# Performance work log

Hardware: AMD Instinct MI355X
Metric: run time of the kernel (lower is better)

## Reference

```python
import jax, jax.numpy as jnp
import numpy as np

B, H, W = 2, 32, 128
HW = H * W
N, C = 4096, 64
KQ, KN = 32, 16          # nsample_q, nsample
DIST = 10.0              # neighbor distance threshold
NEG = -1e10


def _knn(q, p, k):
    # q: (B,M,3), p: (B,N,3) -> idx (B,M,k), sqdist (B,M,k)
    sqd = jnp.sum((q[:, :, None, :] - p[:, None, :, :]) ** 2, axis=-1)
    neg, idx = jax.lax.top_k(-sqd, k)
    return idx, -neg


def _gather(p, idx):
    # p: (B,N,C), idx: (B,M,K) -> (B,M,K,C)
    return jax.vmap(lambda a, i: a[i])(p, idx)


def _norm_feat(x):
    # per-point channel normalization, torch.std default is unbiased (ddof=1)
    m = jnp.mean(x, axis=-1, keepdims=True)
    s = jnp.clip(jnp.std(x, axis=-1, keepdims=True, ddof=1), 1e-12)
    return (x - m) / s


def _conv(x, w, b, g, e):
    # 1x1 conv + BatchNorm (track_running_stats=False -> batch stats) + LeakyReLU(0.1)
    y = jnp.einsum('bnkc,cd->bnkd', x, w) + b
    mu = y.mean(axis=(0, 1, 2), keepdims=True)
    var = y.var(axis=(0, 1, 2), keepdims=True)
    y = (y - mu) * jax.lax.rsqrt(var + 1e-5) * g + e
    return jnp.where(y > 0, y, 0.1 * y)


def setup_inputs() -> dict:
    key = jax.random.key(0)
    ks = jax.random.split(key, 20)
    inp = {
        'xyz_proj_raw': jax.random.normal(ks[0], (B, H, W, 3), jnp.float32),
        'warped_xyz': jax.random.normal(ks[1], (B, HW, 3), jnp.float32),
        'warped_points': jax.random.normal(ks[2], (B, HW, C), jnp.float32),
        'idx_n2': jax.random.randint(ks[3], (B, HW, 2), 0, W),
        'f2_xyz': jax.random.normal(ks[4], (B, N, 3), jnp.float32),
        'f2_points': jax.random.normal(ks[5], (B, N, C), jnp.float32),
        'lidar_z': jax.random.uniform(ks[6], (B, HW, 1), jnp.float32),
    }
    shapes = {
        'm1w0': (70, 128), 'm1w1': (128, 64), 'piw': (6, 64),
        'm2w0': (128, 64), 'm2w1': (64, 64), 'pcw': (10, 64),
        'm3w0': (192, 64), 'm3w1': (64, 64),
    }
    i = 7
    for name, shp in shapes.items():
        inp[name] = jax.random.normal(ks[i], shp, jnp.float32) * 0.05
        i += 1
        pre = name[:-2] if name[-2] == 'w' else name[:-1]
        suf = name[-1] if name[-2] == 'w' else ''
        cout = shp[1]
        inp[pre + 'b' + suf] = jnp.zeros((cout,), jnp.float32)
        inp[pre + 'g' + suf] = jnp.ones((cout,), jnp.float32)
        inp[pre + 'e' + suf] = jnp.zeros((cout,), jnp.float32)
    return inp


def reference(xyz_proj_raw, warped_xyz, warped_points, idx_n2, f2_xyz, f2_points, lidar_z,
              m1w0, m1b0, m1g0, m1e0, m1w1, m1b1, m1g1, m1e1,
              piw, pib, pig, pie,
              m2w0, m2b0, m2g0, m2e0, m2w1, m2b1, m2g1, m2e1,
              pcw, pcb, pcg, pce,
              m3w0, m3b0, m3g0, m3e0, m3w1, m3b1, m3g1, m3e1):
    # ---- stage 1: cross kNN grouping into image features ----
    idx_q, _ = _knn(warped_xyz, f2_xyz, KQ)
    qi_xyz = _gather(f2_xyz, idx_q)          # (B,HW,KQ,3)
    qi_pts = _gather(f2_points, idx_q)       # (B,HW,KQ,C)

    wxyz = warped_xyz * lidar_z              # (B,HW,3)
    pi_xyz_exp = jnp.broadcast_to(wxyz[:, :, None, :], (B, HW, KQ, 3))
    pi_pts_exp = jnp.broadcast_to(warped_points[:, :, None, :], (B, HW, KQ, C))
    pi_xyz_diff_concat = jnp.concatenate([pi_xyz_exp, qi_xyz], axis=3)  # (B,HW,KQ,6)

    pi_feat_diff = _norm_feat(pi_pts_exp) * _norm_feat(qi_pts)          # correlation
    feat = jnp.concatenate([pi_xyz_diff_concat, pi_feat_diff], axis=3)  # (B,HW,KQ,70)

    feat = _conv(feat, m1w0, m1b0, m1g0, m1e0)
    feat = _conv(feat, m1w1, m1b1, m1g1, m1e1)                          # (B,HW,KQ,64)
    pi_enc = _conv(pi_xyz_diff_concat, piw, pib, pig, pie)              # (B,HW,KQ,64)

    pi_cat = jnp.concatenate([pi_enc, feat], axis=3)
    pi_cat = _conv(pi_cat, m2w0, m2b0, m2g0, m2e0)
    pi_cat = _conv(pi_cat, m2w1, m2b1, m2g1, m2e1)
    WQ = jax.nn.softmax(pi_cat, axis=2)
    pi_feat1 = jnp.sum(WQ * feat, axis=2)                               # (B,HW,64)

    # ---- stage 2: self kNN (use_trans=False -> raw projected xyz), thresholded validity ----
    xyz_pr = xyz_proj_raw.reshape(B, HW, 3)
    idx2, sqd2 = _knn(xyz_pr, xyz_pr, KN)
    valid = (sqd2 < DIST * DIST).astype(pi_feat1.dtype)[..., None]      # (B,HW,KN,1)

    pc_xyz_g = _gather(wxyz, idx2)                                      # (B,HW,KN,3)
    pc_pts_g = _gather(pi_feat1, idx2)                                  # (B,HW,KN,64)
    pc_xyz_new = jnp.broadcast_to(wxyz[:, :, None, :], (B, HW, KN, 3))
    pc_pts_new = jnp.broadcast_to(warped_points[:, :, None, :], (B, HW, KN, C))

    pc_diff = pc_xyz_g - pc_xyz_new
    pc_euc = jnp.sqrt(jnp.sum(pc_diff * pc_diff, axis=3, keepdims=True) + 1e-20)
    pc_xyz_cat = jnp.concatenate([pc_xyz_new, pc_xyz_g, pc_diff, pc_euc], axis=3)  # 10ch

    pc_enc = _conv(pc_xyz_cat, pcw, pcb, pcg, pce)
    pc_cat = jnp.concatenate([pc_enc, pc_pts_new, pc_pts_g], axis=-1)   # (B,HW,KN,192)
    pc_cat = _conv(pc_cat, m3w0, m3b0, m3g0, m3e0)
    pc_cat = _conv(pc_cat, m3w1, m3b1, m3g1, m3e1)

    pc_cat = pc_cat * valid + NEG * (1.0 - valid)
    WP = jax.nn.softmax(pc_cat, axis=2)
    out = jnp.sum(WP * pc_pts_g, axis=2)                                # (B,HW,64)
    return out.reshape(B, H, W, -1)
```

## Files before the change

### kernel.cpp

```cpp
#include <hip/hip_runtime.h>
#include <math.h>

constexpr int Bn  = 2;
constexpr int HWn = 4096;
constexpr int Nn  = 4096;
constexpr int KQn = 32;
constexpr int KNn = 16;
constexpr float INV_R1 = 1.0f/262144.0f;
constexpr float INV_R2 = 1.0f/131072.0f;

typedef _Float16 f16x8 __attribute__((ext_vector_type(8)));
typedef float    f32x4 __attribute__((ext_vector_type(4)));

__device__ __forceinline__ float wred64(float v){
  #pragma unroll
  for (int m = 32; m > 0; m >>= 1) v += __shfl_xor(v, m, 64);
  return v;
}
__device__ __forceinline__ float leakyf(float v){ return v > 0.f ? v : 0.1f*v; }

__device__ __forceinline__ void bn_param(const float* st, int c, float inv_n,
                                         const float* g, const float* e,
                                         float& sc, float& sh){
  float mu  = st[c]*inv_n;
  float var = st[128+c]*inv_n - mu*mu;
  float s   = g[c]*rsqrtf(var + 1e-5f);
  sc = s; sh = e[c] - mu*s;
}

__device__ __forceinline__ void build_x70(int row,
    const float* __restrict__ wxyz, const float* __restrict__ f2_xyz,
    const float* __restrict__ normW, const float* __restrict__ normF2,
    const int* __restrict__ idxq, float* x){
  int p = row >> 5;
  int b = p >> 12;
  int idx = idxq[row];
  const float* wx = wxyz + (size_t)p*3;
  const float* fx = f2_xyz + ((size_t)b*Nn + idx)*3;
  x[0]=wx[0]; x[1]=wx[1]; x[2]=wx[2];
  x[3]=fx[0]; x[4]=fx[1]; x[5]=fx[2];
  const float4* nw = (const float4*)(normW  + (size_t)p*64);
  const float4* nf = (const float4*)(normF2 + ((size_t)b*Nn + idx)*64);
  #pragma unroll
  for (int c=0;c<16;c++){
    float4 a = nw[c], q = nf[c];
    x[6+4*c+0]=a.x*q.x; x[6+4*c+1]=a.y*q.y; x[6+4*c+2]=a.z*q.z; x[6+4*c+3]=a.w*q.w;
  }
}

__device__ __forceinline__ void build_x10(int row,
    const float* __restrict__ wxyz, const int* __restrict__ idx2, float* x){
  int p = row >> 4, b = p >> 12;
  int idx = idx2[row];
  const float* nw = wxyz + (size_t)p*3;
  const float* gw = wxyz + ((size_t)b*HWn + idx)*3;
  float n0=nw[0],n1=nw[1],n2=nw[2];
  float g0=gw[0],g1=gw[1],g2=gw[2];
  float d0=g0-n0, d1=g1-n1, d2=g2-n2;
  x[0]=n0;x[1]=n1;x[2]=n2; x[3]=g0;x[4]=g1;x[5]=g2;
  x[6]=d0;x[7]=d1;x[8]=d2; x[9]=sqrtf(d0*d0+d1*d1+d2*d2+1e-20f);
}

__global__ __launch_bounds__(256) void k_prep(
    const float* __restrict__ warped_xyz, const float* __restrict__ lidar_z,
    const float* __restrict__ warped_points, const float* __restrict__ f2_points,
    const float* __restrict__ m1w0, const float* __restrict__ m1w1,
    const float* __restrict__ piw, const float* __restrict__ pcw,
    const float* __restrict__ m2w0, const float* __restrict__ m2w1,
    const float* __restrict__ m3w0, const float* __restrict__ m3w1,
    float* __restrict__ wxyz, float* __restrict__ normW, float* __restrict__ normF2,
    float* __restrict__ piwT, float* __restrict__ pcwT,
    _Float16* __restrict__ w1h, _Float16* __restrict__ w2h,
    _Float16* __restrict__ w3h, _Float16* __restrict__ w4h,
    _Float16* __restrict__ w5h, _Float16* __restrict__ w6h)
{
  int blk = blockIdx.x, tid = threadIdx.x;
  if (blk < 4096){
    int lane = tid & 63;
    int p = blk*4 + (tid >> 6);
    const float* src; float* dst;
    if (p < Bn*HWn){ src = warped_points + (size_t)p*64; dst = normW + (size_t)p*64; }
    else { int q = p - Bn*HWn; src = f2_points + (size_t)q*64; dst = normF2 + (size_t)q*64; }
    float x = src[lane];
    float m = wred64(x) * (1.f/64.f);
    float d = x - m;
    float ss = wred64(d*d);
    float s = fmaxf(sqrtf(ss*(1.f/63.f)), 1e-12f);
    dst[lane] = d / s;
  } else if (blk < 4192){
    int e = (blk-4096)*256 + tid;
    wxyz[e] = warped_xyz[e] * lidar_z[e/3];
  } else if (blk < 4196){
    int e = (blk-4192)*256 + tid;
    if (e < 384){ piwT[(e & 63)*6  + (e >> 6)] = piw[e]; }
    else if (e < 1024){ int f = e-384; pcwT[(f & 63)*10 + (f >> 6)] = pcw[f]; }
  } else {
    int e = (blk-4196)*256 + tid;
    if (e < 12288){
      int j = e/96, k = e - j*96;
      w1h[e] = (k < 70) ? (_Float16)m1w0[k*128 + j] : (_Float16)0.f;
    } else if (e < 20480){
      int f = e - 12288; int d = f >> 7, c = f & 127;
      w2h[f] = (_Float16)m1w1[c*64 + d];
    } else if (e < 28672){
      int f = e - 20480; int d = f >> 7, c = f & 127;
      w3h[f] = (_Float16)m2w0[c*64 + d];
    } else if (e < 32768){
      int f = e - 28672; int d = f >> 6, c = f & 63;
      w4h[f] = (_Float16)m2w1[c*64 + d];
    } else if (e < 45056){
      int f = e - 32768; int d = f/192, c = f - 192*d;
      w5h[f] = (_Float16)m3w0[c*64 + d];
    } else {
      int f = e - 45056; int d = f >> 6, c = f & 63;
      w6h[f] = (_Float16)m3w1[c*64 + d];
    }
  }
}

template<int K, bool WRITE_VALID>
__global__ __launch_bounds__(256) void k_knn(
    const float* __restrict__ qpts, const float* __restrict__ pts,
    int* __restrict__ oidx, float* __restrict__ ovalid)
{
  __shared__ int hist[4*256];
  __shared__ int wsum[4];
  __shared__ unsigned int redm[4], redM[4];
  __shared__ unsigned int sh_sel;
  __shared__ int sh_rem, sh_cls, cnt_lt, cnt_eq;
  int b = blockIdx.x >> 12;
  int qi = blockIdx.x & 4095;
  int tid = threadIdx.x;
  int lane = tid & 63, wv = tid >> 6;
  const float* qp = qpts + ((size_t)(b*HWn+qi))*3;
  float qx=qp[0], qy=qp[1], qz=qp[2];
  const float* pb = pts + (size_t)b*Nn*3;
  unsigned int key[16];
  {
    const float4* pb4 = (const float4*)(pb + (size_t)tid*48);
    float4 v[12];
    #pragma unroll
    for (int i=0;i<12;i++) v[i] = pb4[i];
    const float* f = (const float*)v;
    #pragma unroll
    for (int i=0;i<16;i++){
      float dx = __fsub_rn(qx, f[i*3+0]);
      float dy = __fsub_rn(qy, f[i*3+1]);
      float dz = __fsub_rn(qz, f[i*3+2]);
      float d2 = __fadd_rn(__fadd_rn(__fmul_rn(dx,dx), __fmul_rn(dy,dy)), __fmul_rn(dz,dz));
      key[i] = __float_as_uint(d2);
    }
  }
  unsigned int mn = key[0], mx = key[0];
  #pragma unroll
  for (int i=1;i<16;i++){ mn = min(mn, key[i]); mx = max(mx, key[i]); }
  #pragma unroll
  for (int m=32;m>0;m>>=1){
    mn = min(mn, (unsigned int)__shfl_xor((int)mn, m, 64));
    mx = max(mx, (unsigned int)__shfl_xor((int)mx, m, 64));
  }
  if (lane == 0){ redm[wv] = mn; redM[wv] = mx; }
  if (tid == 0){ cnt_lt = 0; cnt_eq = 0; }
  __syncthreads();
  mn = min(min(redm[0],redm[1]), min(redm[2],redm[3]));
  mx = max(max(redM[0],redM[1]), max(redM[2],redM[3]));
  unsigned int R = mx - mn;
  int L = (R == 0u) ? 0 : (31 - __clz(R));
  int shift = (L > 7) ? (L - 7) : 0;
  unsigned int dmask = 255u;

  unsigned int active = 0xFFFFu, below = 0u;
  int rem = K;
  for (;;){
    __syncthreads();
    #pragma unroll
    for (int j=0;j<4;j++) hist[j*256 + tid] = 0;
    __syncthreads();
    #pragma unroll
    for (int i=0;i<16;i++){
      if (active & (1u<<i))
        atomicAdd(&hist[wv*256 + (int)(((key[i]-mn) >> shift) & dmask)], 1);
    }
    __syncthreads();
    int h = hist[tid] + hist[256+tid] + hist[512+tid] + hist[768+tid];
    int pref = h;
    #pragma unroll
    for (int m=1;m<64;m<<=1){ int t = __shfl_up(pref, m, 64); if (lane >= m) pref += t; }
    if (lane == 63) wsum[wv] = pref;
    __syncthreads();
    int off = 0;
    #pragma unroll
    for (int i=0;i<3;i++) if (i < wv) off += wsum[i];
    pref += off;
    if (pref >= rem && (pref - h) < rem){
      sh_sel = (unsigned int)tid;
      sh_rem = rem - (pref - h);
      sh_cls = h;
    }
    __syncthreads();
    unsigned int sel = sh_sel; rem = sh_rem; int cls = sh_cls;
    #pragma unroll
    for (int i=0;i<16;i++){
      if (active & (1u<<i)){
        unsigned int d = ((key[i]-mn) >> shift) & dmask;
        if (d < sel) below |= (1u<<i);
        if (d != sel) active &= ~(1u<<i);
      }
    }
    if (cls == rem || shift == 0) break;
    int w = (shift < 8) ? shift : 8;
    shift -= w;
    dmask = (w == 8) ? 255u : ((1u<<w) - 1u);
  }
  size_t obase = ((size_t)(b*HWn+qi))*K;
  int nless = K - rem;
  const unsigned int U100 = __float_as_uint(100.0f);
  #pragma unroll
  for (int i=0;i<16;i++){
    if (below & (1u<<i)){
      int s = atomicAdd(&cnt_lt, 1);
      oidx[obase+s] = tid*16 + i;
      if constexpr (WRITE_VALID) ovalid[obase+s] = (key[i] < U100) ? 1.f : 0.f;
    } else if (active & (1u<<i)){
      int s = atomicAdd(&cnt_eq, 1);
      if (s < rem){
        oidx[obase+nless+s] = tid*16 + i;
        if constexpr (WRITE_VALID) ovalid[obase+nless+s] = (key[i] < U100) ? 1.f : 0.f;
      }
    }
  }
}

__global__ __launch_bounds__(256) void k_build_stats(
    const float* __restrict__ wxyz, const float* __restrict__ f2_xyz,
    const float* __restrict__ normW, const float* __restrict__ normF2,
    const int* __restrict__ idxq, const int* __restrict__ idx2,
    const _Float16* __restrict__ w1h,
    _Float16* __restrict__ X1, float* stats, float* __restrict__ gram)
{
  __shared__ float ssum[128], sssq[128];
  __shared__ float sacc[66];
  int blk = blockIdx.x, tid = threadIdx.x, lane = tid & 63;
  if (blk < 1024){
    int row = blk*256 + tid;
    {
      float x[70];
      build_x70(row, wxyz, f2_xyz, normW, normF2, idxq, x);
      unsigned int* d32 = (unsigned int*)(X1 + (size_t)row*96);
      union { unsigned int u; _Float16 h[2]; } pk;
      #pragma unroll
      for (int c=0;c<35;c++){
        pk.h[0] = (_Float16)x[2*c]; pk.h[1] = (_Float16)x[2*c+1];
        d32[c] = pk.u;
      }
      #pragma unroll
      for (int c=35;c<48;c++) d32[c] = 0u;
    }
    if (tid < 128){ ssum[tid]=0.f; sssq[tid]=0.f; }
    __syncthreads();
    int wave = tid >> 6;
    int quad = lane >> 4, n16 = lane & 15;
    float r1[8], r2[8];
    #pragma unroll
    for (int i=0;i<8;i++){ r1[i]=0.f; r2[i]=0.f; }
    for (int t=0;t<4;t++){
      int m0 = blk*256 + t*64 + wave*16;
      const _Float16* xr = X1 + (size_t)(m0 + n16)*96 + quad*8;
      f16x8 a0 = *(const f16x8*)(xr);
      f16x8 a1 = *(const f16x8*)(xr + 32);
      f16x8 a2 = *(const f16x8*)(xr + 64);
      #pragma unroll
      for (int nt = 0; nt < 8; nt++){
        const _Float16* wr = w1h + (size_t)(nt*16 + n16)*96 + quad*8;
        f16x8 b0 = *(const f16x8*)(wr);
        f16x8 b1 = *(const f16x8*)(wr + 32);
        f16x8 b2 = *(const f16x8*)(wr + 64);
        f32x4 acc = {0.f,0.f,0.f,0.f};
        acc = __builtin_amdgcn_mfma_f32_16x16x32_f16(a0, b0, acc, 0,0,0);
        acc = __builtin_amdgcn_mfma_f32_16x16x32_f16(a1, b1, acc, 0,0,0);
        acc = __builtin_amdgcn_mfma_f32_16x16x32_f16(a2, b2, acc, 0,0,0);
        float s1 = acc[0]+acc[1]+acc[2]+acc[3];
        float s2 = acc[0]*acc[0]+acc[1]*acc[1]+acc[2]*acc[2]+acc[3]*acc[3];
        s1 += __shfl_xor(s1, 16, 64); s1 += __shfl_xor(s1, 32, 64);
        s2 += __shfl_xor(s2, 16, 64); s2 += __shfl_xor(s2, 32, 64);
        r1[nt] += s1; r2[nt] += s2;
      }
    }
    if (quad == 0){
      #pragma unroll
      for (int nt=0;nt<8;nt++){
        atomicAdd(&ssum[nt*16+n16], r1[nt]); atomicAdd(&sssq[nt*16+n16], r2[nt]);
      }
    }
    __syncthreads();
    if (tid < 128){ atomicAdd(&stats[tid], ssum[tid]); atomicAdd(&stats[128+tid], sssq[tid]); }
  } else if (blk < 1088){
    float a[28];
    #pragma unroll
    for (int q=0;q<28;q++) a[q]=0.f;
    int g = (blk-1024)*256 + tid;
    for (int s=0;s<16;s++){
      int row = g + s*16384;
      int p = row >> 5, b = p >> 12;
      int idx = idxq[row];
      const float* wx = wxyz + (size_t)p*3;
      const float* fx = f2_xyz + ((size_t)b*Nn + idx)*3;
      float xt[7] = {wx[0],wx[1],wx[2],fx[0],fx[1],fx[2],1.f};
      int q=0;
      #pragma unroll
      for (int i=0;i<7;i++)
        #pragma unroll
        for (int j=i;j<7;j++) a[q++] += xt[i]*xt[j];
    }
    if (tid < 28) sacc[tid]=0.f;
    __syncthreads();
    #pragma unroll
    for (int q=0;q<28;q++){
      float v = wred64(a[q]);
      if (lane==0) atomicAdd(&sacc[q], v);
    }
    __syncthreads();
    if (tid < 28) atomicAdd(&gram[tid], sacc[tid]);
  } else {
    float a[66];
    #pragma unroll
    for (int q=0;q<66;q++) a[q]=0.f;
    int g = (blk-1088)*256 + tid;
    for (int s=0;s<16;s++){
      int row = g + s*8192;
      float x[10];
      build_x10(row, wxyz, idx2, x);
      float xt[11] = {x[0],x[1],x[2],x[3],x[4],x[5],x[6],x[7],x[8],x[9],1.f};
      int q=0;
      #pragma unroll
      for (int i=0;i<11;i++)
        #pragma unroll
        for (int j=i;j<11;j++) a[q++] += xt[i]*xt[j];
    }
    if (tid < 66) sacc[tid]=0.f;
    __syncthreads();
    #pragma unroll
    for (int q=0;q<66;q++){
      float v = wred64(a[q]);
      if (lane==0) atomicAdd(&sacc[q], v);
    }
    __syncthreads();
    if (tid < 66) atomicAdd(&gram[32+tid], sacc[tid]);
  }
}

__global__ __launch_bounds__(128) void k_gram_fin(
    const float* __restrict__ gram,
    const float* __restrict__ piw, const float* __restrict__ pib,
    const float* __restrict__ pcw, const float* __restrict__ pcb,
    float* stats)
{
  int tid = threadIdx.x;
  if (tid < 64){
    int c = tid;
    float wt[7];
    #pragma unroll
    for (int i=0;i<6;i++) wt[i] = piw[i*64+c];
    wt[6] = pib[c];
    const float* G = gram;
    float sum=0.f, ssq=0.f;
    #pragma unroll
    for (int i=0;i<7;i++){
      int offi = i*7 - (i*(i-1))/2;
      sum += wt[i]*G[offi + (6-i)];
      #pragma unroll
      for (int j=0;j<7;j++){
        int ii = i<j? i : j, jj = i<j? j : i;
        int o = ii*7 - (ii*(ii-1))/2 + (jj-ii);
        ssq += wt[i]*wt[j]*G[o];
      }
    }
    stats[2*256+c] = sum; stats[2*256+128+c] = ssq;
  } else {
    int c = tid-64;
    float wt[11];
    #pragma unroll
    for (int i=0;i<10;i++) wt[i] = pcw[i*64+c];
    wt[10] = pcb[c];
    const float* G = gram + 32;
    float sum=0.f, ssq=0.f;
    #pragma unroll
    for (int i=0;i<11;i++){
      int offi = i*11 - (i*(i-1))/2;
      sum += wt[i]*G[offi + (10-i)];
      #pragma unroll
      for (int j=0;j<11;j++){
        int ii = i<j? i : j, jj = i<j? j : i;
        int o = ii*11 - (ii*(ii-1))/2 + (jj-ii);
        ssq += wt[i]*wt[j]*G[o];
      }
    }
    stats[5*256+c] = sum; stats[5*256+128+c] = ssq;
  }
}

__global__ __launch_bounds__(256) void k_mfma_m1(
    const _Float16* __restrict__ X1, const _Float16* __restrict__ w1h,
    const _Float16* __restrict__ w2h,
    const float* __restrict__ m1g0, const float* __restrict__ m1e0,
    float* stats, _Float16* __restrict__ y2h)
{
  __shared__ _Float16 st[64*136];
  __shared__ float sc1[128], sh1[128], ssum[64], sssq[64];
  int tid = threadIdx.x;
  if (tid < 128){
    float s,h; bn_param(stats, tid, INV_R1, m1g0, m1e0, s, h);
    sc1[tid]=s; sh1[tid]=h;
  }
  if (tid < 64){ ssum[tid]=0.f; sssq[tid]=0.f; }
  __syncthreads();
  int wave = tid >> 6, lane = tid & 63;
  int quad = lane >> 4, n16 = lane & 15;
  float r1[4], r2[4];
  #pragma unroll
  for (int i=0;i<4;i++){ r1[i]=0.f; r2[i]=0.f; }
  for (int t=0;t<4;t++){
    int m0 = blockIdx.x*256 + t*64 + wave*16;
    const _Float16* xr = X1 + (size_t)(m0 + n16)*96 + quad*8;
    f16x8 a0 = *(const f16x8*)(xr);
    f16x8 a1 = *(const f16x8*)(xr + 32);
    f16x8 a2 = *(const f16x8*)(xr + 64);
    #pragma unroll
    for (int nt = 0; nt < 8; nt++){
      const _Float16* wr = w1h + (size_t)(nt*16 + n16)*96 + quad*8;
      f16x8 b0 = *(const f16x8*)(wr);
      f16x8 b1 = *(const f16x8*)(wr + 32);
      f16x8 b2 = *(const f16x8*)(wr + 64);
      f32x4 acc = {0.f,0.f,0.f,0.f};
      acc = __builtin_amdgcn_mfma_f32_16x16x32_f16(a0, b0, acc, 0,0,0);
      acc = __builtin_amdgcn_mfma_f32_16x16x32_f16(a1, b1, acc, 0,0,0);
      acc = __builtin_amdgcn_mfma_f32_16x16x32_f16(a2, b2, acc, 0,0,0);
      int ch = nt*16 + n16;
      float sc = sc1[ch], sh = sh1[ch];
      #pragma unroll
      for (int r=0;r<4;r++){
        float v = leakyf(acc[r]*sc + sh);
        st[(size_t)(wave*16 + quad*4 + r)*136 + ch] = (_Float16)v;
      }
    }
    __syncthreads();
    const _Float16* tr = st + (size_t)(wave*16 + n16)*136 + quad*8;
    f16x8 t0 = *(const f16x8*)(tr);
    f16x8 t1 = *(const f16x8*)(tr + 32);
    f16x8 t2 = *(const f16x8*)(tr + 64);
    f16x8 t3 = *(const f16x8*)(tr + 96);
    #pragma unroll
    for (int nt = 0; nt < 4; nt++){
      const _Float16* wr = w2h + (size_t)(nt*16 + n16)*128 + quad*8;
      f16x8 b0 = *(const f16x8*)(wr);
      f16x8 b1 = *(const f16x8*)(wr + 32);
      f16x8 b2 = *(const f16x8*)(wr + 64);
      f16x8 b3 = *(const f16x8*)(wr + 96);
      f32x4 acc = {0.f,0.f,0.f,0.f};
      acc = __builtin_amdgcn_mfma_f32_16x16x32_f16(t0, b0, acc, 0,0,0);
      acc = __builtin_amdgcn_mfma_f32_16x16x32_f16(t1, b1, acc, 0,0,0);
      acc = __builtin_amdgcn_mfma_f32_16x16x32_f16(t2, b2, acc, 0,0,0);
      acc = __builtin_amdgcn_mfma_f32_16x16x32_f16(t3, b3, acc, 0,0,0);
      int ch = nt*16 + n16;
      #pragma unroll
      for (int r=0;r<4;r++){
        int rowg = blockIdx.x*256 + t*64 + wave*16 + quad*4 + r;
        y2h[(size_t)rowg*64 + ch] = (_Float16)acc[r];
      }
      float s1 = acc[0]+acc[1]+acc[2]+acc[3];
      float s2 = acc[0]*acc[0]+acc[1]*acc[1]+acc[2]*acc[2]+acc[3]*acc[3];
      s1 += __shfl_xor(s1, 16, 64); s1 += __shfl_xor(s1, 32, 64);
      s2 += __shfl_xor(s2, 16, 64); s2 += __shfl_xor(s2, 32, 64);
      r1[nt] += s1; r2[nt] += s2;
    }
    __syncthreads();
  }
  if (quad == 0){
    #pragma unroll
    for (int nt=0;nt<4;nt++){
      atomicAdd(&ssum[nt*16+n16], r1[nt]); atomicAdd(&sssq[nt*16+n16], r2[nt]);
    }
  }
  __syncthreads();
  if (tid < 64){ atomicAdd(&stats[1*256+tid], ssum[tid]); atomicAdd(&stats[1*256+128+tid], sssq[tid]); }
}

__global__ __launch_bounds__(256) void k_mfma_m2a(
    const float* __restrict__ wxyz, const float* __restrict__ f2_xyz,
    const int* __restrict__ idxq,
    const float* __restrict__ piwT, const float* __restrict__ pib,
    const float* __restrict__ pig, const float* __restrict__ pie,
    const float* __restrict__ m1g1, const float* __restrict__ m1e1,
    const _Float16* __restrict__ y2h, const _Float16* __restrict__ w3h,
    float* stats, _Float16* __restrict__ y3h)
{
  __shared__ _Float16 su[64*136];
  __shared__ float spw[384];
  __shared__ float scp[64], shp[64], sc2[64], sh2[64], ssum[64], sssq[64];
  int tid = threadIdx.x;
  for (int d = tid; d < 384; d += 256) spw[d] = piwT[d];
  if (tid < 64){
    float s,h;
    bn_param(stats+2*256, tid, INV_R1, pig,  pie,  s, h); scp[tid]=s; shp[tid]=h;
    bn_param(stats+1*256, tid, INV_R1, m1g1, m1e1, s, h); sc2[tid]=s; sh2[tid]=h;
    ssum[tid]=0.f; sssq[tid]=0.f;
  }
  __syncthreads();
  int r = tid & 63, cg = tid >> 6;
  int wave = tid >> 6, lane = tid & 63, quad = lane >> 4, n16 = lane & 15;
  float r1[4], r2[4];
  #pragma unroll
  for (int i=0;i<4;i++){ r1[i]=0.f; r2[i]=0.f; }
  for (int t=0;t<4;t++){
    int rowg = blockIdx.x*256 + t*64 + r;
    {
      int p = rowg >> 5, b = p >> 12;
      int idx = idxq[rowg];
      const float* wx = wxyz + (size_t)p*3;
      const float* fx = f2_xyz + ((size_t)b*Nn + idx)*3;
      float x0=wx[0],x1=wx[1],x2=wx[2],x3=fx[0],x4=fx[1],x5=fx[2];
      #pragma unroll
      for (int jj=0;jj<16;jj++){
        int j = cg*16 + jj;
        const float* pw = spw + j*6;
        float e = pib[j] + x0*pw[0]+x1*pw[1]+x2*pw[2]+x3*pw[3]+x4*pw[4]+x5*pw[5];
        su[r*136 + j] = (_Float16)leakyf(e*scp[j] + shp[j]);
      }
      const f16x8* yr = (const f16x8*)(y2h + (size_t)rowg*64 + cg*16);
      f16x8 q0 = yr[0], q1 = yr[1];
      #pragma unroll
      for (int jj=0;jj<8;jj++){
        int c = cg*16 + jj;
        su[r*136 + 64 + c] = (_Float16)leakyf((float)q0[jj]*sc2[c] + sh2[c]);
      }
      #pragma unroll
      for (int jj=0;jj<8;jj++){
        int c = cg*16 + 8 + jj;
        su[r*136 + 64 + c] = (_Float16)leakyf((float)q1[jj]*sc2[c] + sh2[c]);
      }
    }
    __syncthreads();
    const _Float16* ur = su + (size_t)(wave*16 + n16)*136 + quad*8;
    f16x8 a0 = *(const f16x8*)(ur);
    f16x8 a1 = *(const f16x8*)(ur + 32);
    f16x8 a2 = *(const f16x8*)(ur + 64);
    f16x8 a3 = *(const f16x8*)(ur + 96);
    #pragma unroll
    for (int nt = 0; nt < 4; nt++){
      const _Float16* wr = w3h + (size_t)(nt*16 + n16)*128 + quad*8;
      f16x8 b0 = *(const f16x8*)(wr);
      f16x8 b1 = *(const f16x8*)(wr + 32);
      f16x8 b2 = *(const f16x8*)(wr + 64);
      f16x8 b3 = *(const f16x8*)(wr + 96);
      f32x4 acc = {0.f,0.f,0.f,0.f};
      acc = __builtin_amdgcn_mfma_f32_16x16x32_f16(a0, b0, acc, 0,0,0);
      acc = __builtin_amdgcn_mfma_f32_16x16x32_f16(a1, b1, acc, 0,0,0);
      acc = __builtin_amdgcn_mfma_f32_16x16x32_f16(a2, b2, acc, 0,0,0);
      acc = __builtin_amdgcn_mfma_f32_16x16x32_f16(a3, b3, acc, 0,0,0);
      int ch = nt*16 + n16;
      #pragma unroll
      for (int rr=0;rr<4;rr++){
        int rg = blockIdx.x*256 + t*64 + wave*16 + quad*4 + rr;
        y3h[(size_t)rg*64 + ch] = (_Float16)acc[rr];
      }
      float s1 = acc[0]+acc[1]+acc[2]+acc[3];
      float s2 = acc[0]*acc[0]+acc[1]*acc[1]+acc[2]*acc[2]+acc[3]*acc[3];
      s1 += __shfl_xor(s1, 16, 64); s1 += __shfl_xor(s1, 32, 64);
      s2 += __shfl_xor(s2, 16, 64); s2 += __shfl_xor(s2, 32, 64);
      r1[nt] += s1; r2[nt] += s2;
    }
    __syncthreads();
  }
  if (quad == 0){
    #pragma unroll
    for (int nt=0;nt<4;nt++){
      atomicAdd(&ssum[nt*16+n16], r1[nt]); atomicAdd(&sssq[nt*16+n16], r2[nt]);
    }
  }
  __syncthreads();
  if (tid < 64){ atomicAdd(&stats[3*256+tid], ssum[tid]); atomicAdd(&stats[3*256+128+tid], sssq[tid]); }
}

__global__ __launch_bounds__(256) void k_mfma_pw64(
    const _Float16* __restrict__ yin, const _Float16* __restrict__ wh,
    const float* __restrict__ g, const float* __restrict__ e,
    const float* statsIn, float* statsOut, float inv_n,
    _Float16* __restrict__ yout)
{
  __shared__ _Float16 stt[64*72];
  __shared__ float sc[64], sh[64], ssum[64], sssq[64];
  int tid = threadIdx.x;
  if (tid < 64){
    float s,h; bn_param(statsIn, tid, inv_n, g, e, s, h);
    sc[tid]=s; sh[tid]=h; ssum[tid]=0.f; sssq[tid]=0.f;
  }
  __syncthreads();
  int r = tid & 63, cg = tid >> 6;
  int wave = tid >> 6, lane = tid & 63, quad = lane >> 4, n16 = lane & 15;
  float r1[4], r2[4];
  #pragma unroll
  for (int i=0;i<4;i++){ r1[i]=0.f; r2[i]=0.f; }
  for (int t=0;t<4;t++){
    int rowg = blockIdx.x*256 + t*64 + r;
    const f16x8* yr = (const f16x8*)(yin + (size_t)rowg*64 + cg*16);
    f16x8 q0 = yr[0], q1 = yr[1];
    #pragma unroll
    for (int jj=0;jj<8;jj++){
      int c = cg*16 + jj;
      stt[r*72 + c] = (_Float16)leakyf((float)q0[jj]*sc[c] + sh[c]);
    }
    #pragma unroll
    for (int jj=0;jj<8;jj++){
      int c = cg*16 + 8 + jj;
      stt[r*72 + c] = (_Float16)leakyf((float)q1[jj]*sc[c] + sh[c]);
    }
    __syncthreads();
    const _Float16* tr = stt + (size_t)(wave*16 + n16)*72 + quad*8;
    f16x8 a0 = *(const f16x8*)(tr);
    f16x8 a1 = *(const f16x8*)(tr + 32);
    #pragma unroll
    for (int nt = 0; nt < 4; nt++){
      const _Float16* wr = wh + (size_t)(nt*16 + n16)*64 + quad*8;
      f16x8 b0 = *(const f16x8*)(wr);
      f16x8 b1 = *(const f16x8*)(wr + 32);
      f32x4 acc = {0.f,0.f,0.f,0.f};
      acc = __builtin_amdgcn_mfma_f32_16x16x32_f16(a0, b0, acc, 0,0,0);
      acc = __builtin_amdgcn_mfma_f32_16x16x32_f16(a1, b1, acc, 0,0,0);
      int ch = nt*16 + n16;
      #pragma unroll
      for (int rr=0;rr<4;rr++){
        int rg = blockIdx.x*256 + t*64 + wave*16 + quad*4 + rr;
        yout[(size_t)rg*64 + ch] = (_Float16)acc[rr];
      }
      float s1 = acc[0]+acc[1]+acc[2]+acc[3];
      float s2 = acc[0]*acc[0]+acc[1]*acc[1]+acc[2]*acc[2]+acc[3]*acc[3];
      s1 += __shfl_xor(s1, 16, 64); s1 += __shfl_xor(s1, 32, 64);
      s2 += __shfl_xor(s2, 16, 64); s2 += __shfl_xor(s2, 32, 64);
      r1[nt] += s1; r2[nt] += s2;
    }
    __syncthreads();
  }
  if (quad == 0){
    #pragma unroll
    for (int nt=0;nt<4;nt++){
      atomicAdd(&ssum[nt*16+n16], r1[nt]); atomicAdd(&sssq[nt*16+n16], r2[nt]);
    }
  }
  __syncthreads();
  if (tid < 64){ atomicAdd(&statsOut[tid], ssum[tid]); atomicAdd(&statsOut[128+tid], sssq[tid]); }
}

__global__ __launch_bounds__(256) void k_mfma_m3a(
    const float* __restrict__ wxyz, const float* __restrict__ warped_points,
    const _Float16* __restrict__ pif1h, const int* __restrict__ idx2,
    const float* __restrict__ pcwT, const float* __restrict__ pcb,
    const float* __restrict__ pcg, const float* __restrict__ pce,
    const _Float16* __restrict__ w5h,
    float* stats, _Float16* __restrict__ y5h)
{
  __shared__ _Float16 sv[64*200];
  __shared__ float spw[640];
  __shared__ float scp[64], shp[64], ssum[64], sssq[64];
  int tid = threadIdx.x;
  for (int d = tid; d < 640; d += 256) spw[d] = pcwT[d];
  if (tid < 64){
    float s,h; bn_param(stats+5*256, tid, INV_R2, pcg, pce, s, h);
    scp[tid]=s; shp[tid]=h; ssum[tid]=0.f; sssq[tid]=0.f;
  }
  __syncthreads();
  int r = tid & 63, cg = tid >> 6;
  int wave = tid >> 6, lane = tid & 63, quad = lane >> 4, n16 = lane & 15;
  float r1[4], r2[4];
  #pragma unroll
  for (int i=0;i<4;i++){ r1[i]=0.f; r2[i]=0.f; }
  for (int t=0;t<4;t++){
    int rowg = blockIdx.x*256 + t*64 + r;
    {
      int p = rowg >> 4, b = p >> 12;
      int idx = idx2[rowg];
      float x[10];
      build_x10(rowg, wxyz, idx2, x);
      #pragma unroll
      for (int jj=0;jj<16;jj++){
        int j = cg*16 + jj;
        const float* pw = spw + j*10;
        float e = pcb[j];
        #pragma unroll
        for (int i=0;i<10;i++) e += x[i]*pw[i];
        sv[r*200 + j] = (_Float16)leakyf(e*scp[j] + shp[j]);
      }
      const float4* wp = (const float4*)(warped_points + (size_t)p*64 + cg*16);
      #pragma unroll
      for (int v4=0; v4<4; v4++){
        float4 q = wp[v4];
        int c = 64 + cg*16 + v4*4;
        sv[r*200 + c + 0] = (_Float16)q.x;
        sv[r*200 + c + 1] = (_Float16)q.y;
        sv[r*200 + c + 2] = (_Float16)q.z;
        sv[r*200 + c + 3] = (_Float16)q.w;
      }
      const f16x8* pg = (const f16x8*)(pif1h + ((size_t)(b*HWn) + idx)*64 + cg*16);
      f16x8 g0 = pg[0], g1 = pg[1];
      #pragma unroll
      for (int jj=0;jj<8;jj++) sv[r*200 + 128 + cg*16 + jj] = g0[jj];
      #pragma unroll
      for (int jj=0;jj<8;jj++) sv[r*200 + 136 + cg*16 + jj] = g1[jj];
    }
    __syncthreads();
    const _Float16* vr = sv + (size_t)(wave*16 + n16)*200 + quad*8;
    f16x8 a0 = *(const f16x8*)(vr);
    f16x8 a1 = *(const f16x8*)(vr + 32);
    f16x8 a2 = *(const f16x8*)(vr + 64);
    f16x8 a3 = *(const f16x8*)(vr + 96);
    f16x8 a4 = *(const f16x8*)(vr + 128);
    f16x8 a5 = *(const f16x8*)(vr + 160);
    #pragma unroll
    for (int nt = 0; nt < 4; nt++){
      const _Float16* wr = w5h + (size_t)(nt*16 + n16)*192 + quad*8;
      f32x4 acc = {0.f,0.f,0.f,0.f};
      acc = __builtin_amdgcn_mfma_f32_16x16x32_f16(a0, *(const f16x8*)(wr),       acc, 0,0,0);
      acc = __builtin_amdgcn_mfma_f32_16x16x32_f16(a1, *(const f16x8*)(wr + 32),  acc, 0,0,0);
      acc = __builtin_amdgcn_mfma_f32_16x16x32_f16(a2, *(const f16x8*)(wr + 64),  acc, 0,0,0);
      acc = __builtin_amdgcn_mfma_f32_16x16x32_f16(a3, *(const f16x8*)(wr + 96),  acc, 0,0,0);
      acc = __builtin_amdgcn_mfma_f32_16x16x32_f16(a4, *(const f16x8*)(wr + 128), acc, 0,0,0);
      acc = __builtin_amdgcn_mfma_f32_16x16x32_f16(a5, *(const f16x8*)(wr + 160), acc, 0,0,0);
      int ch = nt*16 + n16;
      #pragma unroll
      for (int rr=0;rr<4;rr++){
        int rg = blockIdx.x*256 + t*64 + wave*16 + quad*4 + rr;
        y5h[(size_t)rg*64 + ch] = (_Float16)acc[rr];
      }
      float s1 = acc[0]+acc[1]+acc[2]+acc[3];
      float s2 = acc[0]*acc[0]+acc[1]*acc[1]+acc[2]*acc[2]+acc[3]*acc[3];
      s1 += __shfl_xor(s1, 16, 64); s1 += __shfl_xor(s1, 32, 64);
      s2 += __shfl_xor(s2, 16, 64); s2 += __shfl_xor(s2, 32, 64);
      r1[nt] += s1; r2[nt] += s2;
    }
    __syncthreads();
  }
  if (quad == 0){
    #pragma unroll
    for (int nt=0;nt<4;nt++){
      atomicAdd(&ssum[nt*16+n16], r1[nt]); atomicAdd(&sssq[nt*16+n16], r2[nt]);
    }
  }
  __syncthreads();
  if (tid < 64){ atomicAdd(&stats[6*256+tid], ssum[tid]); atomicAdd(&stats[6*256+128+tid], sssq[tid]); }
}

__global__ __launch_bounds__(256) void k_softmax1(
    const _Float16* __restrict__ y2h, const _Float16* __restrict__ y4h,
    const float* stats,
    const float* __restrict__ m1g1, const float* __restrict__ m1e1,
    const float* __restrict__ m2g1, const float* __restrict__ m2e1,
    _Float16* __restrict__ pif1h)
{
  int tid = threadIdx.x, lane = tid & 63;
  int p = blockIdx.x*4 + (tid >> 6);
  int d = lane;
  float sc2,sh2,sc4,sh4;
  bn_param(stats+1*256, d, INV_R1, m1g1, m1e1, sc2, sh2);
  bn_param(stats+4*256, d, INV_R1, m2g1, m2e1, sc4, sh4);
  size_t rb = (size_t)p*KQn;
  float v[32]; float mx = -1e30f;
  #pragma unroll
  for (int k=0;k<32;k++){
    float t = leakyf((float)y4h[(rb+k)*64 + d]*sc4 + sh4);
    v[k] = t; mx = fmaxf(mx, t);
  }
  float se = 0.f;
  #pragma unroll
  for (int k=0;k<32;k++){ float ev = __expf(v[k]-mx); v[k]=ev; se += ev; }
  float inv = 1.f/se, acc = 0.f;
  #pragma unroll
  for (int k=0;k<32;k++){
    float f = leakyf((float)y2h[(rb+k)*64 + d]*sc2 + sh2);
    acc += v[k]*f;
  }
  pif1h[(size_t)p*64 + d] = (_Float16)(acc*inv);
}

__global__ __launch_bounds__(256) void k_softmax2(
    const _Float16* __restrict__ y6h, const _Float16* __restrict__ pif1h,
    const int* __restrict__ idx2, const float* __restrict__ validf,
    const float* stats,
    const float* __restrict__ m3g1, const float* __restrict__ m3e1,
    float* __restrict__ out)
{
  int tid = threadIdx.x, lane = tid & 63;
  int p = blockIdx.x*4 + (tid >> 6);
  int b = p >> 12;
  int d = lane;
  float sc,sh; bn_param(stats+7*256, d, INV_R2, m3g1, m3e1, sc, sh);
  size_t rb = (size_t)p*KNn;
  float v[16]; float mx = -1e30f;
  #pragma unroll
  for (int k=0;k<16;k++){
    float t = leakyf((float)y6h[(rb+k)*64 + d]*sc + sh);
    t = (validf[rb+k] > 0.5f) ? t : -1e10f;
    v[k] = t; mx = fmaxf(mx, t);
  }
  float se = 0.f;
  #pragma unroll
  for (int k=0;k<16;k++){ float ev = __expf(v[k]-mx); v[k]=ev; se += ev; }
  float inv = 1.f/se, acc = 0.f;
  #pragma unroll
  for (int k=0;k<16;k++){
    int idx = idx2[rb+k];
    acc += v[k]*(float)pif1h[((size_t)(b*HWn) + idx)*64 + d];
  }
  out[(size_t)p*64 + d] = acc*inv;
}

extern "C" void kernel_launch(void* const* d_in, const int* in_sizes, int n_in,
                              void* d_out, int out_size, void* d_ws, size_t ws_size,
                              hipStream_t stream)
{
  (void)in_sizes; (void)n_in; (void)out_size; (void)ws_size;
  const float* xyz_proj      = (const float*)d_in[0];
  const float* warped_xyz    = (const float*)d_in[1];
  const float* warped_points = (const float*)d_in[2];
  const float* f2_xyz        = (const float*)d_in[4];
  const float* f2_points     = (const float*)d_in[5];
  const float* lidar_z       = (const float*)d_in[6];
  const float* m1w0=(const float*)d_in[7],  *m1g0=(const float*)d_in[9],  *m1e0=(const float*)d_in[10];
  const float* m1w1=(const float*)d_in[11], *m1g1=(const float*)d_in[13], *m1e1=(const float*)d_in[14];
  const float* piw =(const float*)d_in[15], *pib =(const float*)d_in[16], *pig =(const float*)d_in[17], *pie =(const float*)d_in[18];
  const float* m2w0=(const float*)d_in[19], *m2g0=(const float*)d_in[21], *m2e0=(const float*)d_in[22];
  const float* m2w1=(const float*)d_in[23], *m2g1=(const float*)d_in[25], *m2e1=(const float*)d_in[26];
  const float* pcw =(const float*)d_in[27], *pcb =(const float*)d_in[28], *pcg =(const float*)d_in[29], *pce =(const float*)d_in[30];
  const float* m3w0=(const float*)d_in[31], *m3g0=(const float*)d_in[33], *m3e0=(const float*)d_in[34];
  const float* m3w1=(const float*)d_in[35], *m3g1=(const float*)d_in[37], *m3e1=(const float*)d_in[38];
  float* out = (float*)d_out;

  float* ws     = (float*)d_ws;
  float* wxyz   = ws;
  float* normW  = wxyz   + 24576;
  float* normF2 = normW  + 524288;
  float* piwT   = normF2 + 524288;
  float* pcwT   = piwT   + 384;
  float* stats  = pcwT   + 640;
  float* gram   = stats  + 2048;
  int*   idxq   = (int*)(gram + 128);
  int*   idx2   = idxq   + 262144;
  float* validf = (float*)(idx2 + 131072);
  _Float16* pif1h = (_Float16*)(validf + 131072);
  float* X1f    = validf + 131072 + 524288;
  _Float16* X1  = (_Float16*)X1f;
  float* y2f    = X1f + 12582912;
  _Float16* y2h = (_Float16*)y2f;
  float* y3f    = y2f + 8388608;
  _Float16* y3h = (_Float16*)y3f;
  float* whb    = y3f + 8388608;
  _Float16* w1h = (_Float16*)whb;
  _Float16* w2h = w1h + 12288;
  _Float16* w3h = w2h + 8192;
  _Float16* w4h = w3h + 8192;
  _Float16* w5h = w4h + 4096;
  _Float16* w6h = w5h + 12288;
  _Float16* y4h = (_Float16*)X1f;
  _Float16* y5h = (_Float16*)(X1f + 8388608);
  _Float16* y6h = y3h;

  hipMemsetAsync(stats, 0, (2048+128)*sizeof(float), stream);
  k_prep<<<4388,256,0,stream>>>(warped_xyz, lidar_z, warped_points, f2_points,
                                m1w0, m1w1, piw, pcw, m2w0, m2w1, m3w0, m3w1,
                                wxyz, normW, normF2, piwT, pcwT,
                                w1h, w2h, w3h, w4h, w5h, w6h);
  k_knn<32,false><<<8192,256,0,stream>>>(warped_xyz, f2_xyz, idxq, nullptr);
  k_knn<16,true ><<<8192,256,0,stream>>>(xyz_proj, xyz_proj, idx2, validf);
  k_build_stats<<<1120,256,0,stream>>>(wxyz, f2_xyz, normW, normF2, idxq, idx2,
                                       w1h, X1, stats, gram);
  k_gram_fin<<<1,128,0,stream>>>(gram, piw, pib, pcw, pcb, stats);
  k_mfma_m1<<<1024,256,0,stream>>>(X1, w1h, w2h, m1g0, m1e0, stats, y2h);
  k_mfma_m2a<<<1024,256,0,stream>>>(wxyz, f2_xyz, idxq, piwT, pib, pig, pie,
                                    m1g1, m1e1, y2h, w3h, stats, y3h);
  k_mfma_pw64<<<1024,256,0,stream>>>(y3h, w4h, m2g0, m2e0,
                                     stats+3*256, stats+4*256, INV_R1, y4h);
  k_softmax1<<<2048,256,0,stream>>>(y2h, y4h, stats, m1g1, m1e1, m2g1, m2e1, pif1h);
  k_mfma_m3a<<<512,256,0,stream>>>(wxyz, warped_points, pif1h, idx2,
                                   pcwT, pcb, pcg, pce, w5h, stats, y5h);
  k_mfma_pw64<<<512,256,0,stream>>>(y5h, w6h, m3g0, m3e0,
                                    stats+6*256, stats+7*256, INV_R2, y6h);
  k_softmax2<<<2048,256,0,stream>>>(y6h, pif1h, idx2, validf, stats, m3g1, m3e1, out);
}
```

Before: 548.3 us.

## Merge both KNN launches and use a 12-bit first radix-select pass

```diff
diff --git a/kernel.cpp b/kernel.cpp
--- a/kernel.cpp
+++ b/kernel.cpp
@@ -118,18 +118,23 @@
   }
 }
 
-template<int K, bool WRITE_VALID>
-__global__ __launch_bounds__(256) void k_knn(
-    const float* __restrict__ qpts, const float* __restrict__ pts,
-    int* __restrict__ oidx, float* __restrict__ ovalid)
-{
-  __shared__ int hist[4*256];
+__global__ __launch_bounds__(256) void k_knn_all(
+    const float* __restrict__ qA, const float* __restrict__ pA, int* __restrict__ oA,
+    const float* __restrict__ qB, const float* __restrict__ pB, int* __restrict__ oB,
+    float* __restrict__ ovalid)
+{
+  __shared__ int hist[4096];
   __shared__ int wsum[4];
   __shared__ unsigned int redm[4], redM[4];
-  __shared__ unsigned int sh_sel;
-  __shared__ int sh_rem, sh_cls, cnt_lt, cnt_eq;
-  int b = blockIdx.x >> 12;
-  int qi = blockIdx.x & 4095;
+  __shared__ int sh_sel, sh_rem, sh_cls, cnt_lt, cnt_eq;
+  bool second = blockIdx.x >= 8192;
+  int blk = second ? (blockIdx.x - 8192) : blockIdx.x;
+  int K = second ? KNn : KQn;
+  const float* qpts = second ? qB : qA;
+  const float* pts  = second ? pB : pA;
+  int* oidx = second ? oB : oA;
+  int b = blk >> 12;
+  int qi = blk & 4095;
   int tid = threadIdx.x;
   int lane = tid & 63, wv = tid >> 6;
   const float* qp = qpts + ((size_t)(b*HWn+qi))*3;
@@ -166,39 +171,75 @@
   mx = max(max(redM[0],redM[1]), max(redM[2],redM[3]));
   unsigned int R = mx - mn;
   int L = (R == 0u) ? 0 : (31 - __clz(R));
-  int shift = (L > 7) ? (L - 7) : 0;
-  unsigned int dmask = 255u;
+  int shift = (L > 11) ? (L - 11) : 0;
+  unsigned int dmask = 4095u;
 
   unsigned int active = 0xFFFFu, below = 0u;
   int rem = K;
+  bool first = true;
   for (;;){
     __syncthreads();
-    #pragma unroll
-    for (int j=0;j<4;j++) hist[j*256 + tid] = 0;
+    if (first){
+      int4 z = {0,0,0,0};
+      #pragma unroll
+      for (int j=0;j<4;j++) ((int4*)hist)[tid + j*256] = z;
+    } else {
+      hist[tid] = 0;
+    }
     __syncthreads();
     #pragma unroll
     for (int i=0;i<16;i++){
       if (active & (1u<<i))
-        atomicAdd(&hist[wv*256 + (int)(((key[i]-mn) >> shift) & dmask)], 1);
-    }
-    __syncthreads();
-    int h = hist[tid] + hist[256+tid] + hist[512+tid] + hist[768+tid];
-    int pref = h;
-    #pragma unroll
-    for (int m=1;m<64;m<<=1){ int t = __shfl_up(pref, m, 64); if (lane >= m) pref += t; }
-    if (lane == 63) wsum[wv] = pref;
-    __syncthreads();
-    int off = 0;
-    #pragma unroll
-    for (int i=0;i<3;i++) if (i < wv) off += wsum[i];
-    pref += off;
-    if (pref >= rem && (pref - h) < rem){
-      sh_sel = (unsigned int)tid;
-      sh_rem = rem - (pref - h);
-      sh_cls = h;
-    }
-    __syncthreads();
-    unsigned int sel = sh_sel; rem = sh_rem; int cls = sh_cls;
+        atomicAdd(&hist[(int)(((key[i]-mn) >> shift) & dmask)], 1);
+    }
+    __syncthreads();
+    if (first){
+      int base = tid*16;
+      int hv[16]; int tot = 0;
+      #pragma unroll
+      for (int i=0;i<16;i++){ hv[i] = hist[base+i]; tot += hv[i]; }
+      int pref = tot;
+      #pragma unroll
+      for (int m=1;m<64;m<<=1){ int t = __shfl_up(pref, m, 64); if (lane >= m) pref += t; }
+      if (lane == 63) wsum[wv] = pref;
+      __syncthreads();
+      int off = 0;
+      #pragma unroll
+      for (int i=0;i<3;i++) if (i < wv) off += wsum[i];
+      pref += off;
+      if (pref >= rem && (pref - tot) < rem){
+        int running = pref - tot;
+        bool done = false;
+        #pragma unroll
+        for (int i=0;i<16;i++){
+          if (!done && running + hv[i] >= rem){
+            sh_sel = base + i;
+            sh_rem = rem - running;
+            sh_cls = hv[i];
+            done = true;
+          }
+          if (!done) running += hv[i];
+        }
+      }
+    } else {
+      int h = hist[tid];
+      int pref = h;
+      #pragma unroll
+      for (int m=1;m<64;m<<=1){ int t = __shfl_up(pref, m, 64); if (lane >= m) pref += t; }
+      if (lane == 63) wsum[wv] = pref;
+      __syncthreads();
+      int off = 0;
+      #pragma unroll
+      for (int i=0;i<3;i++) if (i < wv) off += wsum[i];
+      pref += off;
+      if (pref >= rem && (pref - h) < rem){
+        sh_sel = tid;
+        sh_rem = rem - (pref - h);
+        sh_cls = h;
+      }
+    }
+    __syncthreads();
+    unsigned int sel = (unsigned int)sh_sel; rem = sh_rem; int cls = sh_cls;
     #pragma unroll
     for (int i=0;i<16;i++){
       if (active & (1u<<i)){
@@ -211,6 +252,7 @@
     int w = (shift < 8) ? shift : 8;
     shift -= w;
     dmask = (w == 8) ? 255u : ((1u<<w) - 1u);
+    first = false;
   }
   size_t obase = ((size_t)(b*HWn+qi))*K;
   int nless = K - rem;
@@ -220,12 +262,12 @@
     if (below & (1u<<i)){
       int s = atomicAdd(&cnt_lt, 1);
       oidx[obase+s] = tid*16 + i;
-      if constexpr (WRITE_VALID) ovalid[obase+s] = (key[i] < U100) ? 1.f : 0.f;
+      if (second) ovalid[obase+s] = (key[i] < U100) ? 1.f : 0.f;
     } else if (active & (1u<<i)){
       int s = atomicAdd(&cnt_eq, 1);
       if (s < rem){
         oidx[obase+nless+s] = tid*16 + i;
-        if constexpr (WRITE_VALID) ovalid[obase+nless+s] = (key[i] < U100) ? 1.f : 0.f;
+        if (second) ovalid[obase+nless+s] = (key[i] < U100) ? 1.f : 0.f;
       }
     }
   }
@@ -867,8 +909,8 @@
                                 m1w0, m1w1, piw, pcw, m2w0, m2w1, m3w0, m3w1,
                                 wxyz, normW, normF2, piwT, pcwT,
                                 w1h, w2h, w3h, w4h, w5h, w6h);
-  k_knn<32,false><<<8192,256,0,stream>>>(warped_xyz, f2_xyz, idxq, nullptr);
-  k_knn<16,true ><<<8192,256,0,stream>>>(xyz_proj, xyz_proj, idx2, validf);
+  k_knn_all<<<16384,256,0,stream>>>(warped_xyz, f2_xyz, idxq,
+                                    xyz_proj, xyz_proj, idx2, validf);
   k_build_stats<<<1120,256,0,stream>>>(wxyz, f2_xyz, normW, normF2, idxq, idx2,
                                        w1h, X1, stats, gram);
   k_gram_fin<<<1,128,0,stream>>>(gram, piw, pib, pcw, pcb, stats);
```

Measured after the change: 516.2 us, median of 3. 5.9% less time.
